# Kernel optimization log

Measured on AMD Instinct MI355X. Metric: run time of the kernel, lower is better.

Reference implementation:

```python
import jax, jax.numpy as jnp
import numpy as np

B, T, C, K, NC = 256, 240, 512, 64, 4  # batch, chunk_size, dim, clusters, num_classes+1
EPS = 1e-12


def setup_inputs() -> dict:
    key = jax.random.key(0)
    k1, k2, k3, k4 = jax.random.split(key, 4)
    inputs = jax.random.normal(k1, (B, T, C), dtype=jnp.float32)
    conv_w = jax.random.normal(k2, (K, C), dtype=jnp.float32) * 0.05   # 1x1 assignment conv, no bias (vladv2=False)
    centroids = jax.random.normal(k3, (K, C), dtype=jnp.float32)
    fc_w = jax.random.normal(k4, (NC, K * C), dtype=jnp.float32) * 0.02
    fc_b = jnp.zeros((NC,), dtype=jnp.float32)
    return {"inputs": inputs, "conv_w": conv_w, "centroids": centroids, "fc_w": fc_w, "fc_b": fc_b}


def _l2norm(x, axis):
    return x / jnp.clip(jnp.linalg.norm(x, axis=axis, keepdims=True), EPS)


def reference(inputs, conv_w, centroids, fc_w, fc_b):
    # inputs: [B, T, C]. Torch permutes to NCHW=(B, C, T, 1); feature dim = C.
    x = _l2norm(inputs, axis=-1)                      # normalize_input over feature dim
    # soft assignment: 1x1 conv -> logits [B, T, K], softmax over clusters
    a = jax.nn.softmax(jnp.einsum('btc,kc->btk', x, conv_w), axis=-1)
    # vlad[b,k,c] = sum_t a[b,t,k] * (x[b,t,c] - centroids[k,c])
    #            = einsum(a, x) - (sum_t a) * centroids   (avoids [B,K,C,T] intermediate)
    vlad = jnp.einsum('btk,btc->bkc', a, x) - a.sum(axis=1)[:, :, None] * centroids[None]
    vlad = _l2norm(vlad, axis=-1)                     # intra-normalization over C
    v = vlad.reshape(vlad.shape[0], -1)               # [B, K*C]
    v = _l2norm(v, axis=-1)                           # final L2 normalize
    # dropout is identity in eval mode; fc + sigmoid
    return jax.nn.sigmoid(v @ fc_w.T + fc_b)
```

## Files before the change

kernel.cpp:

```cpp
#include <hip/hip_runtime.h>
#include <hip/hip_bf16.h>
#include <stdint.h>

#define BB 256
#define TT 240
#define CC 512
#define KK 64
#define NCLS 4
#define CHUNK 32
#define NCHUNK 8
#define THREADS 512

typedef __attribute__((ext_vector_type(8))) short bf16x8;
typedef __attribute__((ext_vector_type(4))) float f32x4;

__device__ __forceinline__ float u2f(unsigned int u) {
    union { unsigned int i; float f; } x; x.i = u; return x.f;
}
__device__ __forceinline__ unsigned short f2bf(float f) {
    union { float f; unsigned int i; } x; x.f = f;
    unsigned int r = x.i + 0x7FFFu + ((x.i >> 16) & 1u);
    return (unsigned short)(r >> 16);
}
__device__ __forceinline__ unsigned int pk2(float lo, float hi) {
    return ((unsigned int)f2bf(hi) << 16) | (unsigned int)f2bf(lo);
}

struct alignas(16) SMemChunk {
    unsigned short x[CHUNK][520];
    unsigned short xT[CC][40];
    float logitsA[CHUNK][65];
    unsigned short aT[KK][40];
};
struct alignas(16) SMemEpi { unsigned short vbuf[KK * CC]; };
union SMemU { SMemChunk c; SMemEpi e; };

__global__ __launch_bounds__(THREADS, 2) void netvlad_kernel(
    const float* __restrict__ inp,
    const float* __restrict__ convw,
    const float* __restrict__ cent,
    const float* __restrict__ fcw,
    const float* __restrict__ fcb,
    float* __restrict__ out)
{
    __shared__ SMemU sm;
    __shared__ float asum[KK];
    __shared__ float ssred[2][KK];
    __shared__ float gred[8];
    __shared__ float fcred[8][NCLS];
    __shared__ float vinv_sh;

    const int tid  = threadIdx.x;
    const int b    = blockIdx.x;
    const int w    = tid >> 6;
    const int lane = tid & 63;
    const int grp  = (lane >> 4) & 3;
    const int col  = lane & 15;
    const int w2   = w >> 1;
    const int half = w & 1;

    if (tid < KK) asum[tid] = 0.f;

    f32x4 acc[16];
    #pragma unroll
    for (int j = 0; j < 16; ++j) acc[j] = (f32x4){0.f, 0.f, 0.f, 0.f};

    bf16x8 cw[16];
    #pragma unroll
    for (int ks = 0; ks < 16; ++ks) {
        const float* p = convw + (size_t)(w2 * 16 + col) * CC + ks * 32 + grp * 8;
        float4 a0 = *(const float4*)p;
        float4 a1 = *(const float4*)(p + 4);
        bf16x8 v;
        v[0] = (short)f2bf(a0.x); v[1] = (short)f2bf(a0.y);
        v[2] = (short)f2bf(a0.z); v[3] = (short)f2bf(a0.w);
        v[4] = (short)f2bf(a1.x); v[5] = (short)f2bf(a1.y);
        v[6] = (short)f2bf(a1.z); v[7] = (short)f2bf(a1.w);
        cw[ks] = v;
    }

    const size_t ibase = (size_t)b * (TT * CC);

    uint4 pf[4];
    #pragma unroll
    for (int i = 0; i < 4; ++i) {
        int g = tid + i * THREADS;
        int t = g >> 6, c8 = (g & 63) << 3;
        const float* p = inp + ibase + (size_t)t * CC + c8;
        float4 u0 = *(const float4*)p;
        float4 u1 = *(const float4*)(p + 4);
        pf[i] = (uint4){pk2(u0.x, u0.y), pk2(u0.z, u0.w), pk2(u1.x, u1.y), pk2(u1.z, u1.w)};
    }

    for (int ch = 0; ch < NCHUNK; ++ch) {
        const int t0 = ch * CHUNK;
        const int tvalid = (TT - t0 < CHUNK) ? (TT - t0) : CHUNK;

        __syncthreads();

        #pragma unroll
        for (int i = 0; i < 4; ++i) {
            int g = tid + i * THREADS;
            int t = g >> 6, c8 = (g & 63) << 3;
            uint4 val = pf[i];
            if (t >= tvalid) val = (uint4){0u, 0u, 0u, 0u};
            *(uint4*)&sm.c.x[t][c8] = val;
        }
        if (ch + 1 < NCHUNK) {
            int nt0 = t0 + CHUNK;
            #pragma unroll
            for (int i = 0; i < 4; ++i) {
                int g = tid + i * THREADS;
                int t = g >> 6, c8 = (g & 63) << 3;
                int gt = nt0 + t; if (gt > TT - 1) gt = TT - 1;
                const float* p = inp + ibase + (size_t)gt * CC + c8;
                float4 u0 = *(const float4*)p;
                float4 u1 = *(const float4*)(p + 4);
                pf[i] = (uint4){pk2(u0.x, u0.y), pk2(u0.z, u0.w), pk2(u1.x, u1.y), pk2(u1.z, u1.w)};
            }
        }
        __syncthreads();

        {
            int c = tid;
            #pragma unroll
            for (int tb = 0; tb < 4; ++tb) {
                bf16x8 v;
                #pragma unroll
                for (int j = 0; j < 8; ++j) v[j] = (short)sm.c.x[tb * 8 + j][c];
                *(bf16x8*)&sm.c.xT[c][tb * 8] = v;
            }
        }

        {
            f32x4 lt = (f32x4){0.f, 0.f, 0.f, 0.f};
            #pragma unroll
            for (int ks = 0; ks < 16; ++ks) {
                bf16x8 bb = *(const bf16x8*)&sm.c.x[half * 16 + col][ks * 32 + grp * 8];
                lt = __builtin_amdgcn_mfma_f32_16x16x32_bf16(cw[ks], bb, lt, 0, 0, 0);
            }
            #pragma unroll
            for (int r = 0; r < 4; ++r)
                sm.c.logitsA[half * 16 + col][w2 * 16 + grp * 4 + r] = lt[r];
        }
        __syncthreads();

        {
            int t = tid >> 4, part = tid & 15;
            float ssp = 0.f;
            #pragma unroll
            for (int k = 0; k < 4; ++k) {
                uint4 u4 = *(const uint4*)&sm.c.x[t][part * 32 + k * 8];
                const unsigned int* pu = (const unsigned int*)&u4;
                #pragma unroll
                for (int h = 0; h < 4; ++h) {
                    unsigned int u = pu[h];
                    float lo = u2f(u << 16), hi = u2f(u & 0xFFFF0000u);
                    ssp += lo * lo + hi * hi;
                }
            }
            ssp += __shfl_xor(ssp, 1); ssp += __shfl_xor(ssp, 2);
            ssp += __shfl_xor(ssp, 4); ssp += __shfl_xor(ssp, 8);
            float rinv = 1.f / fmaxf(sqrtf(ssp), 1e-12f);
            rinv = (t < tvalid) ? rinv : 0.f;

            float l[4]; float lmax = -1e30f;
            #pragma unroll
            for (int q = 0; q < 4; ++q) {
                l[q] = sm.c.logitsA[t][q * 16 + part] * rinv;
                lmax = fmaxf(lmax, l[q]);
            }
            lmax = fmaxf(lmax, __shfl_xor(lmax, 1));
            lmax = fmaxf(lmax, __shfl_xor(lmax, 2));
            lmax = fmaxf(lmax, __shfl_xor(lmax, 4));
            lmax = fmaxf(lmax, __shfl_xor(lmax, 8));
            float es = 0.f;
            #pragma unroll
            for (int q = 0; q < 4; ++q) { l[q] = __expf(l[q] - lmax); es += l[q]; }
            es += __shfl_xor(es, 1); es += __shfl_xor(es, 2);
            es += __shfl_xor(es, 4); es += __shfl_xor(es, 8);
            float is = 1.f / es;
            #pragma unroll
            for (int q = 0; q < 4; ++q) {
                float a = l[q] * is;
                sm.c.logitsA[t][q * 16 + part] = a;
                sm.c.aT[q * 16 + part][t] = (unsigned short)f2bf(a * rinv);
            }
        }
        __syncthreads();

        if (tid < KK) {
            float s = 0.f;
            for (int t = 0; t < tvalid; ++t) s += sm.c.logitsA[t][tid];
            asum[tid] += s;
        }

        {
            bf16x8 af = *(const bf16x8*)&sm.c.aT[w2 * 16 + col][grp * 8];
            #pragma unroll
            for (int j = 0; j < 16; ++j) {
                bf16x8 bf = *(const bf16x8*)&sm.c.xT[half * 256 + j * 16 + col][grp * 8];
                acc[j] = __builtin_amdgcn_mfma_f32_16x16x32_bf16(af, bf, acc[j], 0, 0, 0);
            }
        }
    }

    __syncthreads();

    #pragma unroll
    for (int r = 0; r < 4; ++r) {
        int cl = w2 * 16 + grp * 4 + r;
        float as = asum[cl];
        float ss = 0.f;
        #pragma unroll
        for (int j = 0; j < 16; ++j) {
            int c = half * 256 + j * 16 + col;
            float v = acc[j][r] - as * cent[(size_t)cl * CC + c];
            acc[j][r] = v;
            ss += v * v;
        }
        ss += __shfl_xor(ss, 1); ss += __shfl_xor(ss, 2);
        ss += __shfl_xor(ss, 4); ss += __shfl_xor(ss, 8);
        if (col == 0) ssred[half][cl] = ss;
    }
    __syncthreads();

    float contrib = 0.f;
    #pragma unroll
    for (int r = 0; r < 4; ++r) {
        int cl = w2 * 16 + grp * 4 + r;
        float ss = ssred[0][cl] + ssred[1][cl];
        float inv = 1.f / fmaxf(sqrtf(ss), 1e-12f);
        #pragma unroll
        for (int j = 0; j < 16; ++j) {
            float v = acc[j][r] * inv;
            acc[j][r] = v;
            contrib += v * v;
        }
    }
    #pragma unroll
    for (int m = 1; m < 64; m <<= 1) contrib += __shfl_xor(contrib, m);
    if (lane == 0) gred[w] = contrib;
    __syncthreads();
    if (tid == 0) {
        float tot = 0.f;
        #pragma unroll
        for (int i = 0; i < 8; ++i) tot += gred[i];
        vinv_sh = 1.f / fmaxf(sqrtf(tot), 1e-12f);
    }
    __syncthreads();

    {
        float vinv = vinv_sh;
        #pragma unroll
        for (int r = 0; r < 4; ++r) {
            int cl = w2 * 16 + grp * 4 + r;
            #pragma unroll
            for (int j = 0; j < 16; ++j) {
                int c = half * 256 + j * 16 + col;
                sm.e.vbuf[cl * CC + c] = f2bf(acc[j][r] * vinv);
            }
        }
    }
    __syncthreads();

    float pacc[NCLS] = {0.f, 0.f, 0.f, 0.f};
    #pragma unroll
    for (int i = 0; i < 8; ++i) {
        int idx = i * 4096 + tid * 8;
        bf16x8 vv = *(const bf16x8*)&sm.e.vbuf[idx];
        float vf[8];
        #pragma unroll
        for (int h = 0; h < 8; ++h) {
            union { unsigned int u; float f; } cvt;
            cvt.u = ((unsigned int)(unsigned short)vv[h]) << 16;
            vf[h] = cvt.f;
        }
        #pragma unroll
        for (int nc = 0; nc < NCLS; ++nc) {
            const float* wp = fcw + (size_t)nc * (KK * CC) + idx;
            float4 w0 = *(const float4*)wp;
            float4 w1 = *(const float4*)(wp + 4);
            pacc[nc] += vf[0] * w0.x + vf[1] * w0.y + vf[2] * w0.z + vf[3] * w0.w
                      + vf[4] * w1.x + vf[5] * w1.y + vf[6] * w1.z + vf[7] * w1.w;
        }
    }
    #pragma unroll
    for (int nc = 0; nc < NCLS; ++nc) {
        #pragma unroll
        for (int m = 1; m < 64; m <<= 1) pacc[nc] += __shfl_xor(pacc[nc], m);
    }
    if (lane == 0) {
        #pragma unroll
        for (int nc = 0; nc < NCLS; ++nc) fcred[w][nc] = pacc[nc];
    }
    __syncthreads();
    if (tid < NCLS) {
        float s = fcb[tid];
        #pragma unroll
        for (int ww = 0; ww < 8; ++ww) s += fcred[ww][tid];
        out[b * NCLS + tid] = 1.f / (1.f + __expf(-s));
    }
}

extern "C" void kernel_launch(void* const* d_in, const int* in_sizes, int n_in,
                              void* d_out, int out_size, void* d_ws, size_t ws_size,
                              hipStream_t stream) {
    const float* inp   = (const float*)d_in[0];
    const float* convw = (const float*)d_in[1];
    const float* cent  = (const float*)d_in[2];
    const float* fcw   = (const float*)d_in[3];
    const float* fcb   = (const float*)d_in[4];
    float* o = (float*)d_out;
    netvlad_kernel<<<BB, THREADS, 0, stream>>>(inp, convw, cent, fcw, fcb, o);
}
```

Before: 215.0 us.

## Overlap input prefetch with barriers and compute row norms from fp32 staging

Prefetch registers now hold raw fp32 values. Conversion to bf16 is deferred to the store stage, which also computes each row's sum of squares with wave shuffles into shared memory, replacing the later recompute from bf16 LDS. __syncthreads is replaced by an inline s_waitcnt lgkmcnt(0)+s_barrier, so barriers no longer wait for outstanding global prefetch loads, and the redundant top-of-loop barrier is removed. This doubles the prefetch register footprint, which risks spills under the 2-blocks-per-CU launch bound. Norms now come from fp32 rather than bf16 values.

Result: faster. 206.2 us (-4.1%).

```diff
diff --git a/kernel.cpp b/kernel.cpp
--- a/kernel.cpp
+++ b/kernel.cpp
@@ -14,9 +14,6 @@
 typedef __attribute__((ext_vector_type(8))) short bf16x8;
 typedef __attribute__((ext_vector_type(4))) float f32x4;
 
-__device__ __forceinline__ float u2f(unsigned int u) {
-    union { unsigned int i; float f; } x; x.i = u; return x.f;
-}
 __device__ __forceinline__ unsigned short f2bf(float f) {
     union { float f; unsigned int i; } x; x.f = f;
     unsigned int r = x.i + 0x7FFFu + ((x.i >> 16) & 1u);
@@ -24,6 +21,9 @@
 }
 __device__ __forceinline__ unsigned int pk2(float lo, float hi) {
     return ((unsigned int)f2bf(hi) << 16) | (unsigned int)f2bf(lo);
+}
+__device__ __forceinline__ void LB() {
+    asm volatile("s_waitcnt lgkmcnt(0)\n\ts_barrier" ::: "memory");
 }
 
 struct alignas(16) SMemChunk {
@@ -44,6 +44,7 @@
     float* __restrict__ out)
 {
     __shared__ SMemU sm;
+    __shared__ float sumsq_sh[CHUNK];
     __shared__ float asum[KK];
     __shared__ float ssred[2][KK];
     __shared__ float gred[8];
@@ -81,30 +82,34 @@
 
     const size_t ibase = (size_t)b * (TT * CC);
 
-    uint4 pf[4];
+    float4 r0[4], r1[4];
     #pragma unroll
     for (int i = 0; i < 4; ++i) {
         int g = tid + i * THREADS;
         int t = g >> 6, c8 = (g & 63) << 3;
         const float* p = inp + ibase + (size_t)t * CC + c8;
-        float4 u0 = *(const float4*)p;
-        float4 u1 = *(const float4*)(p + 4);
-        pf[i] = (uint4){pk2(u0.x, u0.y), pk2(u0.z, u0.w), pk2(u1.x, u1.y), pk2(u1.z, u1.w)};
+        r0[i] = *(const float4*)p;
+        r1[i] = *(const float4*)(p + 4);
     }
 
     for (int ch = 0; ch < NCHUNK; ++ch) {
         const int t0 = ch * CHUNK;
         const int tvalid = (TT - t0 < CHUNK) ? (TT - t0) : CHUNK;
 
-        __syncthreads();
-
         #pragma unroll
         for (int i = 0; i < 4; ++i) {
             int g = tid + i * THREADS;
             int t = g >> 6, c8 = (g & 63) << 3;
-            uint4 val = pf[i];
-            if (t >= tvalid) val = (uint4){0u, 0u, 0u, 0u};
+            float4 u0 = r0[i], u1 = r1[i];
+            uint4 val = (uint4){pk2(u0.x, u0.y), pk2(u0.z, u0.w),
+                                pk2(u1.x, u1.y), pk2(u1.z, u1.w)};
+            float s = u0.x*u0.x + u0.y*u0.y + u0.z*u0.z + u0.w*u0.w
+                    + u1.x*u1.x + u1.y*u1.y + u1.z*u1.z + u1.w*u1.w;
+            if (t >= tvalid) { val = (uint4){0u,0u,0u,0u}; s = 0.f; }
             *(uint4*)&sm.c.x[t][c8] = val;
+            s += __shfl_xor(s, 1);  s += __shfl_xor(s, 2);  s += __shfl_xor(s, 4);
+            s += __shfl_xor(s, 8);  s += __shfl_xor(s, 16); s += __shfl_xor(s, 32);
+            if (lane == 0) sumsq_sh[t] = s;
         }
         if (ch + 1 < NCHUNK) {
             int nt0 = t0 + CHUNK;
@@ -114,12 +119,11 @@
                 int t = g >> 6, c8 = (g & 63) << 3;
                 int gt = nt0 + t; if (gt > TT - 1) gt = TT - 1;
                 const float* p = inp + ibase + (size_t)gt * CC + c8;
-                float4 u0 = *(const float4*)p;
-                float4 u1 = *(const float4*)(p + 4);
-                pf[i] = (uint4){pk2(u0.x, u0.y), pk2(u0.z, u0.w), pk2(u1.x, u1.y), pk2(u1.z, u1.w)};
-            }
-        }
-        __syncthreads();
+                r0[i] = *(const float4*)p;
+                r1[i] = *(const float4*)(p + 4);
+            }
+        }
+        LB();
 
         {
             int c = tid;
@@ -143,25 +147,11 @@
             for (int r = 0; r < 4; ++r)
                 sm.c.logitsA[half * 16 + col][w2 * 16 + grp * 4 + r] = lt[r];
         }
-        __syncthreads();
+        LB();
 
         {
             int t = tid >> 4, part = tid & 15;
-            float ssp = 0.f;
-            #pragma unroll
-            for (int k = 0; k < 4; ++k) {
-                uint4 u4 = *(const uint4*)&sm.c.x[t][part * 32 + k * 8];
-                const unsigned int* pu = (const unsigned int*)&u4;
-                #pragma unroll
-                for (int h = 0; h < 4; ++h) {
-                    unsigned int u = pu[h];
-                    float lo = u2f(u << 16), hi = u2f(u & 0xFFFF0000u);
-                    ssp += lo * lo + hi * hi;
-                }
-            }
-            ssp += __shfl_xor(ssp, 1); ssp += __shfl_xor(ssp, 2);
-            ssp += __shfl_xor(ssp, 4); ssp += __shfl_xor(ssp, 8);
-            float rinv = 1.f / fmaxf(sqrtf(ssp), 1e-12f);
+            float rinv = 1.f / fmaxf(sqrtf(sumsq_sh[t]), 1e-12f);
             rinv = (t < tvalid) ? rinv : 0.f;
 
             float l[4]; float lmax = -1e30f;
@@ -187,7 +177,7 @@
                 sm.c.aT[q * 16 + part][t] = (unsigned short)f2bf(a * rinv);
             }
         }
-        __syncthreads();
+        LB();
 
         if (tid < KK) {
             float s = 0.f;
@@ -205,7 +195,7 @@
         }
     }
 
-    __syncthreads();
+    LB();
 
     #pragma unroll
     for (int r = 0; r < 4; ++r) {
@@ -223,7 +213,7 @@
         ss += __shfl_xor(ss, 4); ss += __shfl_xor(ss, 8);
         if (col == 0) ssred[half][cl] = ss;
     }
-    __syncthreads();
+    LB();
 
     float contrib = 0.f;
     #pragma unroll
@@ -241,14 +231,14 @@
     #pragma unroll
     for (int m = 1; m < 64; m <<= 1) contrib += __shfl_xor(contrib, m);
     if (lane == 0) gred[w] = contrib;
-    __syncthreads();
+    LB();
     if (tid == 0) {
         float tot = 0.f;
         #pragma unroll
         for (int i = 0; i < 8; ++i) tot += gred[i];
         vinv_sh = 1.f / fmaxf(sqrtf(tot), 1e-12f);
     }
-    __syncthreads();
+    LB();
 
     {
         float vinv = vinv_sh;
@@ -262,7 +252,7 @@
             }
         }
     }
-    __syncthreads();
+    LB();
 
     float pacc[NCLS] = {0.f, 0.f, 0.f, 0.f};
     #pragma unroll
@@ -294,7 +284,7 @@
         #pragma unroll
         for (int nc = 0; nc < NCLS; ++nc) fcred[w][nc] = pacc[nc];
     }
-    __syncthreads();
+    LB();
     if (tid < NCLS) {
         float s = fcb[tid];
         #pragma unroll
```
